# Performance work log

Hardware: AMD Instinct MI355X
Metric: run time of the kernel (lower is better)

## Reference

```python
import jax, jax.numpy as jnp
import numpy as np

LN_EPS = 1e-5

def _prelu(x, a):
    return jnp.where(x > 0, x, a * x)

def setup_inputs() -> dict:
    key = jax.random.key(0)
    ks = jax.random.split(key, 16)
    C, NH, HD = 256, 8, 32
    s = lambda k, shape, scale: jax.random.normal(k, shape, jnp.float32) * scale
    return {
        "x":   s(ks[0], (1, C, 48, 48), 1.0),
        "Wq":  s(ks[1], (NH, HD, C), 1.0 / np.sqrt(C)),
        "bq":  s(ks[2], (NH, HD), 0.02),
        "Wk":  s(ks[3], (NH, HD, C), 1.0 / np.sqrt(C)),
        "bk":  s(ks[4], (NH, HD), 0.02),
        "Wv":  s(ks[5], (NH, HD, C), 1.0 / np.sqrt(C)),
        "bv":  s(ks[6], (NH, HD), 0.02),
        "Wfc": s(ks[7], (C, C), 1.0 / np.sqrt(C)),
        "bfc": s(ks[8], (C,), 0.02),
        "w1":  s(ks[9], (C // 16, C), 1.0 / np.sqrt(C)),
        "b1":  s(ks[10], (C // 16,), 0.02),
        "a1":  jnp.full((1,), 0.25, jnp.float32),
        "w2":  s(ks[11], (C, C // 16), 1.0 / np.sqrt(C // 16)),
        "b2":  s(ks[12], (C,), 0.02),
        "a2":  jnp.full((1,), 0.25, jnp.float32),
    }

def _mha(xs, Wq, bq, Wk, bk, Wv, bv, Wfc, bfc):
    # xs: [B, C, Hs, Ws]; all heads batched into one einsum per projection
    B, C, Hs, Ws = xs.shape
    N = Hs * Ws
    xf = xs.reshape(B, C, N)
    q = jnp.einsum('bcn,hdc->bhnd', xf, Wq) + bq[None, :, None, :]
    k = jnp.einsum('bcn,hdc->bhnd', xf, Wk) + bk[None, :, None, :]
    v = jnp.einsum('bcn,hdc->bhnd', xf, Wv) + bv[None, :, None, :]
    # unscaled scores, softmax over keys (matches torch.bmm(q,k) + softmax dim=-1)
    attn = jax.nn.softmax(jnp.einsum('bhnd,bhmd->bhnm', q, k), axis=-1)
    o = jnp.einsum('bhnm,bhmd->bhnd', attn, v)          # [B, H, N, D]
    o = o.transpose(0, 1, 3, 2).reshape(B, C, Hs, Ws)   # concat heads along C
    return jnp.einsum('bchw,oc->bohw', o, Wfc) + bfc[None, :, None, None]

def reference(x, Wq, bq, Wk, bk, Wv, bv, Wfc, bfc, w1, b1, a1, w2, b2, a2):
    B, C, H, W = x.shape
    num_scales = 4
    out = jnp.zeros_like(x)
    for i in range(num_scales):
        Hs, Ws = H // (2 ** i), W // (2 ** i)
        xs = jax.image.resize(x, (B, C, Hs, Ws), 'bilinear', antialias=False)
        y = _mha(xs, Wq, bq, Wk, bk, Wv, bv, Wfc, bfc)
        out = out + jax.image.resize(y, (B, C, H, W), 'bilinear', antialias=False)
    # SE channel gating
    avg = out.mean(axis=(2, 3))                         # [B, C]
    h = _prelu(avg @ w1.T + b1, a1)
    cw = jax.nn.sigmoid(h @ w2.T + b2)                  # [B, C]
    out = out * cw[:, :, None, None] + x
    # layer_norm over (C, H, W), no affine
    mu = out.mean(axis=(1, 2, 3), keepdims=True)
    var = out.var(axis=(1, 2, 3), keepdims=True)
    out = (out - mu) * jax.lax.rsqrt(var + LN_EPS)
    out = _prelu(out, a2)
    # dropout is identity in eval mode
    return out
```

## Files before the change

kernel.cpp:

```cpp
#include <hip/hip_runtime.h>
#include <hip/hip_bf16.h>

#define NTOT 3060
#define NPIX 2304
#define CH   256
#define NLN  589824
#define VSTR 3072

#define P0_OFF   0
#define P1_OFF   2359296
#define PM0_OFF  2654208
#define PL0_OFF  2727936
#define PM1_OFF  2801664
#define PL1_OFF  2810880

typedef __attribute__((ext_vector_type(8))) short bf16x8;
typedef __attribute__((ext_vector_type(16))) float f32x16;

__device__ __forceinline__ bf16x8 ldfrag(const unsigned short* p) {
  int4 v = *reinterpret_cast<const int4*>(p);
  return __builtin_bit_cast(bf16x8, v);
}
__device__ __forceinline__ unsigned f2bf(float f) {
  unsigned u = __builtin_bit_cast(unsigned, f);
  return (u + 0x7FFFu + ((u >> 16) & 1u)) >> 16;
}
__device__ __forceinline__ unsigned pk2(float a, float b) {
  return f2bf(a) | (f2bf(b) << 16);
}
#define MFMA32(a, b, c) __builtin_amdgcn_mfma_f32_32x32x16_bf16((a), (b), (c), 0, 0, 0)

__global__ __launch_bounds__(256) void k_downsample(const float* __restrict__ x,
                                                    float* __restrict__ xs) {
  int idx = blockIdx.x * 256 + threadIdx.x;
  if (idx >= CH * NTOT) return;
  int c = idx / NTOT;
  int n = idx - c * NTOT;
  const float* xc = x + c * NPIX;
  int p, Ws, s;
  if (n < 2304)      { s = 0; p = n;        Ws = 48; }
  else if (n < 2880) { s = 1; p = n - 2304; Ws = 24; }
  else if (n < 3024) { s = 2; p = n - 2880; Ws = 12; }
  else               { s = 3; p = n - 3024; Ws = 6;  }
  int oy = p / Ws, ox = p - oy * Ws;
  float v;
  if (s == 0) {
    v = xc[p];
  } else {
    int r, cc;
    if (s == 1)      { r = 2 * oy;     cc = 2 * ox;     }
    else if (s == 2) { r = 4 * oy + 1; cc = 4 * ox + 1; }
    else             { r = 8 * oy + 3; cc = 8 * ox + 3; }
    v = 0.25f * (xc[r * 48 + cc] + xc[r * 48 + cc + 1] +
                 xc[(r + 1) * 48 + cc] + xc[(r + 1) * 48 + cc + 1]);
  }
  xs[idx] = v;
}

__global__ __launch_bounds__(256) void k_gemm256(
    const float* __restrict__ A0, const float* __restrict__ A1, const float* __restrict__ A2,
    const float* __restrict__ b0, const float* __restrict__ b1, const float* __restrict__ b2,
    const float* __restrict__ Bm,
    float* __restrict__ O0, float* __restrict__ O1, float* __restrict__ O2) {
  int z = blockIdx.z;
  const float* A    = (z == 0) ? A0 : (z == 1) ? A1 : A2;
  const float* bias = (z == 0) ? b0 : (z == 1) ? b1 : b2;
  float* OUT        = (z == 0) ? O0 : (z == 1) ? O1 : O2;

  __shared__ float As[16][68];
  __shared__ float Bs[16][68];

  int t  = threadIdx.x;
  int j0 = blockIdx.y * 64, n0 = blockIdx.x * 64;
  int ty = t >> 4, tx = t & 15;
  int arow = t >> 2, acol4 = (t & 3) * 4;
  int nn = t & 63, kkb = t >> 6;

  float acc[4][4];
#pragma unroll
  for (int i = 0; i < 4; i++)
#pragma unroll
    for (int q = 0; q < 4; q++) acc[i][q] = 0.f;

  for (int k0 = 0; k0 < 256; k0 += 16) {
    float4 av = *(const float4*)&A[(j0 + arow) * 256 + k0 + acol4];
    float bstage[4];
#pragma unroll
    for (int r = 0; r < 4; r++) {
      int kk = kkb + r * 4;
      int n = n0 + nn;
      bstage[r] = (n < NTOT) ? Bm[(k0 + kk) * NTOT + n] : 0.f;
    }
    __syncthreads();
    As[acol4 + 0][arow] = av.x;
    As[acol4 + 1][arow] = av.y;
    As[acol4 + 2][arow] = av.z;
    As[acol4 + 3][arow] = av.w;
#pragma unroll
    for (int r = 0; r < 4; r++) Bs[kkb + r * 4][nn] = bstage[r];
    __syncthreads();
#pragma unroll
    for (int kk = 0; kk < 16; kk++) {
      float4 a = *(const float4*)&As[kk][ty * 4];
      float4 b = *(const float4*)&Bs[kk][tx * 4];
      float avv[4] = {a.x, a.y, a.z, a.w};
      float bvv[4] = {b.x, b.y, b.z, b.w};
#pragma unroll
      for (int i = 0; i < 4; i++)
#pragma unroll
        for (int q = 0; q < 4; q++) acc[i][q] += avv[i] * bvv[q];
    }
  }
#pragma unroll
  for (int i = 0; i < 4; i++) {
    int j = j0 + ty * 4 + i;
    float bb = bias[j];
#pragma unroll
    for (int q = 0; q < 4; q++) {
      int n = n0 + tx * 4 + q;
      if (n < NTOT) OUT[j * NTOT + n] = acc[i][q] + bb;
    }
  }
}

__global__ __launch_bounds__(256) void k_repackT(const float* __restrict__ Qb,
                                                 const float* __restrict__ Kb,
                                                 unsigned short* __restrict__ Qbf,
                                                 unsigned short* __restrict__ Kbf) {
  __shared__ float Ls[32][65];
  int t = threadIdx.x;
  int n0 = blockIdx.x * 64;
  int h  = blockIdx.y;
  const float* src = (blockIdx.z == 0) ? Qb : Kb;
  unsigned short* dst = (blockIdx.z == 0) ? Qbf : Kbf;
#pragma unroll
  for (int i = 0; i < 8; i++) {
    int idx = t + i * 256;
    int d = idx >> 6, tk = idx & 63;
    int n = n0 + tk;
    Ls[d][tk] = (n < NTOT) ? src[(h * 32 + d) * NTOT + n] : 0.f;
  }
  __syncthreads();
  int tk = t >> 2, dq = t & 3;
  int n = n0 + tk;
  if (n < NTOT) {
    unsigned w[4];
#pragma unroll
    for (int j = 0; j < 4; j++)
      w[j] = pk2(Ls[dq * 8 + 2 * j][tk], Ls[dq * 8 + 2 * j + 1][tk]);
    int4 out = make_int4((int)w[0], (int)w[1], (int)w[2], (int)w[3]);
    *reinterpret_cast<int4*>(&dst[((size_t)h * NTOT + n) * 32 + dq * 8]) = out;
  }
}

__global__ __launch_bounds__(256) void k_castV(const float* __restrict__ Vb,
                                               unsigned short* __restrict__ Vt) {
  int row = blockIdx.x;
  int t = threadIdx.x;
  for (int i = 0; i < 3; i++) {
    int c4 = t + i * 256;
    if (c4 < 765) {
      float4 v = *(const float4*)&Vb[(size_t)row * NTOT + c4 * 4];
      unsigned u0 = pk2(v.x, v.y), u1 = pk2(v.z, v.w);
      int2 out = make_int2((int)u0, (int)u1);
      *reinterpret_cast<int2*>(&Vt[(size_t)row * VSTR + c4 * 4]) = out;
    }
  }
}

__global__ __launch_bounds__(256) void k_attn_mfma(const unsigned short* __restrict__ Qbf,
                                                   const unsigned short* __restrict__ Kbf,
                                                   const unsigned short* __restrict__ Vt,
                                                   float* __restrict__ Ob,
                                                   float* __restrict__ Pb) {
  const int Ns_tab[4]  = {2304, 576, 144, 36};
  const int off_tab[4] = {0, 2304, 2880, 3024};

  int bid = blockIdx.x;
  int sc, head, qt, sp, nsp;
  if (bid < 576)      { int qtb = bid >> 2; sp = bid & 3;  nsp = 4; sc = 0; head = qtb / 18; qt = qtb - head * 18; }
  else if (bid < 656) { int b = bid - 576; int qtb = b >> 1; sp = b & 1; nsp = 2; sc = 1; head = qtb / 5; qt = qtb - head * 5; }
  else if (bid < 672) { int b = bid - 656; sc = 2; head = b >> 1; qt = b & 1; sp = 0; nsp = 1; }
  else                { sc = 3; head = bid - 672; qt = 0; sp = 0; nsp = 1; }

  int Ns = Ns_tab[sc], off = off_tab[sc];
  int t = threadIdx.x;
  int w = t >> 6, l = t & 63;
  int lq = l & 31, h2 = l >> 5;
  int qbase = qt * 128 + w * 32;
  if (qbase >= Ns) return;

  int chunk = Ns / nsp;
  int kbeg = sp * chunk, kend = kbeg + chunk;

  const unsigned short* Qh = Qbf + ((size_t)head * NTOT + off) * 32;
  const unsigned short* Kh = Kbf + ((size_t)head * NTOT + off) * 32;
  const unsigned short* Vh = Vt + (size_t)(head * 32) * VSTR + off;

  int qc = qbase + lq; if (qc >= Ns) qc = Ns - 1;
  const unsigned short* Qp = Qh + (size_t)qc * 32 + h2 * 8;
  bf16x8 qf0 = ldfrag(Qp);
  bf16x8 qf1 = ldfrag(Qp + 16);

  float m = -3.0e38f, L = 0.f;
  f32x16 oacc = {0,0,0,0,0,0,0,0,0,0,0,0,0,0,0,0};

  int mt0 = kbeg + lq; if (mt0 >= Ns) mt0 = Ns - 1;
  const unsigned short* Kp0 = Kh + (size_t)mt0 * 32 + h2 * 8;
  bf16x8 kf0n = ldfrag(Kp0);
  bf16x8 kf1n = ldfrag(Kp0 + 16);

  for (int kb = kbeg; kb < kend; kb += 32) {
    bf16x8 kf0 = kf0n, kf1 = kf1n;
    const unsigned short* Vp = Vh + (size_t)lq * VSTR + kb + h2 * 8;
    bf16x8 vf0 = ldfrag(Vp);
    bf16x8 vf1 = ldfrag(Vp + 16);
    int kb2 = kb + 32;
    if (kb2 < kend) {
      int mt = kb2 + lq; if (mt >= Ns) mt = Ns - 1;
      const unsigned short* Kp = Kh + (size_t)mt * 32 + h2 * 8;
      kf0n = ldfrag(Kp);
      kf1n = ldfrag(Kp + 16);
    }

    f32x16 sa = {0,0,0,0,0,0,0,0,0,0,0,0,0,0,0,0};
    sa = MFMA32(kf0, qf0, sa);
    sa = MFMA32(kf1, qf1, sa);

    float s[16];
#pragma unroll
    for (int r = 0; r < 16; r++) s[r] = sa[r];
    int rem = kend - kb;
    if (rem < 32) {
#pragma unroll
      for (int r = 0; r < 16; r++) {
        int ko = (r & 3) + 8 * (r >> 2) + 4 * h2;
        if (ko >= rem) s[r] = -3.0e38f;
      }
    }
    float cm = s[0];
#pragma unroll
    for (int r = 1; r < 16; r++) cm = fmaxf(cm, s[r]);
    cm = fmaxf(cm, __shfl_xor(cm, 32));
    float mn = fmaxf(m, cm);
    float scl = __expf(m - mn);
    m = mn;
    L *= scl;
#pragma unroll
    for (int r = 0; r < 16; r++) oacc[r] *= scl;

    float p[16], ls = 0.f;
#pragma unroll
    for (int r = 0; r < 16; r++) { p[r] = __expf(s[r] - m); ls += p[r]; }
    ls += __shfl_xor(ls, 32);
    L += ls;

    unsigned u[8], su[8];
#pragma unroll
    for (int g = 0; g < 8; g++) u[g] = pk2(p[2 * g], p[2 * g + 1]);
#pragma unroll
    for (int g = 0; g < 8; g++) su[g] = __shfl_xor(u[g], 32);

    int4 w0, w1;
    if (h2 == 0) {
      w0 = make_int4((int)u[0], (int)u[1], (int)su[0], (int)su[1]);
      w1 = make_int4((int)u[4], (int)u[5], (int)su[4], (int)su[5]);
    } else {
      w0 = make_int4((int)su[2], (int)su[3], (int)u[2], (int)u[3]);
      w1 = make_int4((int)su[6], (int)su[7], (int)u[6], (int)u[7]);
    }
    bf16x8 pf0 = __builtin_bit_cast(bf16x8, w0);
    bf16x8 pf1 = __builtin_bit_cast(bf16x8, w1);

    oacc = MFMA32(vf0, pf0, oacc);
    oacc = MFMA32(vf1, pf1, oacc);
  }

  int q = qbase + lq;
  if (q < Ns) {
    if (nsp == 1) {
      float rl = 1.f / L;
      float* Op = Ob + (size_t)(head * 32) * NTOT + off + q;
#pragma unroll
      for (int r = 0; r < 16; r++) {
        int dr = (r & 3) + 8 * (r >> 2) + 4 * h2;
        Op[(size_t)dr * NTOT] = oacc[r] * rl;
      }
    } else {
      int qs = (sc == 0) ? 2304 : 576;
      float* P  = (sc == 0) ? Pb + P0_OFF  : Pb + P1_OFF;
      float* Pm = (sc == 0) ? Pb + PM0_OFF : Pb + PM1_OFF;
      float* PL = (sc == 0) ? Pb + PL0_OFF : Pb + PL1_OFF;
      size_t row = (size_t)(sp * 8 + head) * qs + q;
      float* Prow = P + row * 32;
#pragma unroll
      for (int g = 0; g < 4; g++) {
        float4 v = make_float4(oacc[4 * g + 0], oacc[4 * g + 1],
                               oacc[4 * g + 2], oacc[4 * g + 3]);
        *(float4*)&Prow[g * 8 + 4 * h2] = v;
      }
      if (h2 == 0) { Pm[row] = m; PL[row] = L; }
    }
  }
}

__global__ __launch_bounds__(256) void k_combine(const float* __restrict__ Pb,
                                                 float* __restrict__ Ob) {
  int tid = blockIdx.x * 256 + threadIdx.x;
  int h, q, off, nsp, qs;
  const float* P; const float* Pm; const float* PL;
  if (tid < 18432) {
    h = tid / 2304; q = tid - h * 2304; off = 0; nsp = 4; qs = 2304;
    P = Pb + P0_OFF; Pm = Pb + PM0_OFF; PL = Pb + PL0_OFF;
  } else if (tid < 23040) {
    int b = tid - 18432;
    h = b / 576; q = b - h * 576; off = 2304; nsp = 2; qs = 576;
    P = Pb + P1_OFF; Pm = Pb + PM1_OFF; PL = Pb + PL1_OFF;
  } else return;

  float mv[4], lv[4];
  float M = -3.0e38f;
  for (int s = 0; s < nsp; s++) {
    size_t row = (size_t)(s * 8 + h) * qs + q;
    mv[s] = Pm[row]; lv[s] = PL[row];
    M = fmaxf(M, mv[s]);
  }
  float e[4], denom = 0.f;
  for (int s = 0; s < nsp; s++) { e[s] = __expf(mv[s] - M); denom += e[s] * lv[s]; }
  float rden = 1.f / denom;

  float* Op = Ob + (size_t)(h * 32) * NTOT + off + q;
#pragma unroll
  for (int d4 = 0; d4 < 8; d4++) {
    float4 acc = make_float4(0.f, 0.f, 0.f, 0.f);
    for (int s = 0; s < nsp; s++) {
      size_t row = (size_t)(s * 8 + h) * qs + q;
      float4 v = *(const float4*)&P[row * 32 + d4 * 4];
      acc.x += e[s] * v.x; acc.y += e[s] * v.y;
      acc.z += e[s] * v.z; acc.w += e[s] * v.w;
    }
    Op[(size_t)(d4 * 4 + 0) * NTOT] = acc.x * rden;
    Op[(size_t)(d4 * 4 + 1) * NTOT] = acc.y * rden;
    Op[(size_t)(d4 * 4 + 2) * NTOT] = acc.z * rden;
    Op[(size_t)(d4 * 4 + 3) * NTOT] = acc.w * rden;
  }
}

__device__ __forceinline__ float bil4(const float* __restrict__ a, int S,
                                      int y, int x, float scale, float tr) {
  float fy = fmaf((float)y, scale, tr);
  float fx = fmaf((float)x, scale, tr);
  int iy = (int)floorf(fy); float wy = fy - (float)iy;
  int ix = (int)floorf(fx); float wx = fx - (float)ix;
  int y0 = min(max(iy, 0), S - 1);
  int y1 = min(max(iy + 1, 0), S - 1);
  int x0 = min(max(ix, 0), S - 1);
  int x1 = min(max(ix + 1, 0), S - 1);
  float v00 = a[y0 * S + x0], v01 = a[y0 * S + x1];
  float v10 = a[y1 * S + x0], v11 = a[y1 * S + x1];
  float top = v00 + wx * (v01 - v00);
  float bot = v10 + wx * (v11 - v10);
  return top + wy * (bot - top);
}

__global__ __launch_bounds__(256) void k_upacc(const float* __restrict__ Y,
                                               float* __restrict__ outa) {
  int idx = blockIdx.x * 256 + threadIdx.x;
  if (idx >= NLN) return;
  int c = idx / NPIX;
  int p = idx - c * NPIX;
  int y = p / 48, x = p - y * 48;
  const float* Yc = Y + c * NTOT;
  float v = Yc[p];
  v += bil4(Yc + 2304, 24, y, x, 0.5f,   -0.25f);
  v += bil4(Yc + 2880, 12, y, x, 0.25f,  -0.375f);
  v += bil4(Yc + 3024, 6,  y, x, 0.125f, -0.4375f);
  outa[idx] = v;
}

__global__ __launch_bounds__(256) void k_chanstats(const float* __restrict__ outa,
                                                   const float* __restrict__ x,
                                                   float* __restrict__ st) {
  int c = blockIdx.x, t = threadIdx.x;
  float so = 0.f, soo = 0.f, sox = 0.f, sx = 0.f, sxx = 0.f;
  for (int p = t; p < NPIX; p += 256) {
    float o  = outa[c * NPIX + p];
    float xv = x[c * NPIX + p];
    so += o; soo += o * o; sox += o * xv; sx += xv; sxx += xv * xv;
  }
#pragma unroll
  for (int off = 32; off > 0; off >>= 1) {
    so  += __shfl_down(so, off, 64);
    soo += __shfl_down(soo, off, 64);
    sox += __shfl_down(sox, off, 64);
    sx  += __shfl_down(sx, off, 64);
    sxx += __shfl_down(sxx, off, 64);
  }
  __shared__ float part[4][5];
  int wv = t >> 6;
  if ((t & 63) == 0) {
    part[wv][0] = so; part[wv][1] = soo; part[wv][2] = sox;
    part[wv][3] = sx; part[wv][4] = sxx;
  }
  __syncthreads();
  if (t == 0) {
    float a0 = 0.f, a1 = 0.f, a2 = 0.f, a3 = 0.f, a4 = 0.f;
#pragma unroll
    for (int wi = 0; wi < 4; wi++) {
      a0 += part[wi][0]; a1 += part[wi][1]; a2 += part[wi][2];
      a3 += part[wi][3]; a4 += part[wi][4];
    }
    st[c] = a0; st[256 + c] = a1; st[512 + c] = a2; st[768 + c] = a3; st[1024 + c] = a4;
  }
}

__global__ __launch_bounds__(256) void k_se(const float* __restrict__ st,
                                            const float* __restrict__ w1,
                                            const float* __restrict__ b1,
                                            const float* __restrict__ a1,
                                            const float* __restrict__ w2,
                                            const float* __restrict__ b2,
                                            float* __restrict__ cw,
                                            float* __restrict__ scal) {
  __shared__ float avg_s[256];
  __shared__ float h_s[16];
  __shared__ float rS[4], rSS[4];
  int t = threadIdx.x;
  float avg = st[t] * (1.f / (float)NPIX);
  avg_s[t] = avg;
  __syncthreads();
  int i = t >> 4, pp = t & 15;
  float partial = 0.f;
  for (int c = pp; c < 256; c += 16) partial += avg_s[c] * w1[i * 256 + c];
#pragma unroll
  for (int off = 8; off > 0; off >>= 1) partial += __shfl_down(partial, off, 16);
  if (pp == 0) {
    float hv = partial + b1[i];
    float al = a1[0];
    h_s[i] = hv > 0.f ? hv : al * hv;
  }
  __syncthreads();
  float s2 = b2[t];
#pragma unroll
  for (int k = 0; k < 16; k++) s2 += h_s[k] * w2[t * 16 + k];
  float cwv = 1.f / (1.f + expf(-s2));
  cw[t] = cwv;

  float S_part  = cwv * st[t] + st[768 + t];
  float SS_part = cwv * cwv * st[256 + t] + 2.f * cwv * st[512 + t] + st[1024 + t];
#pragma unroll
  for (int off = 32; off > 0; off >>= 1) {
    S_part  += __shfl_down(S_part, off, 64);
    SS_part += __shfl_down(SS_part, off, 64);
  }
  if ((t & 63) == 0) { rS[t >> 6] = S_part; rSS[t >> 6] = SS_part; }
  __syncthreads();
  if (t == 0) {
    float S = rS[0] + rS[1] + rS[2] + rS[3];
    float SS = rSS[0] + rSS[1] + rSS[2] + rSS[3];
    float mu = S / (float)NLN;
    float var = SS / (float)NLN - mu * mu;
    scal[0] = mu;
    scal[1] = rsqrtf(var + 1e-5f);
  }
}

__global__ __launch_bounds__(256) void k_final(const float* __restrict__ outa,
                                               const float* __restrict__ x,
                                               const float* __restrict__ cw,
                                               const float* __restrict__ scal,
                                               const float* __restrict__ a2,
                                               float* __restrict__ out) {
  int idx = blockIdx.x * 256 + threadIdx.x;
  if (idx >= NLN) return;
  int c = idx / NPIX;
  float g = outa[idx] * cw[c] + x[idx];
  float v = (g - scal[0]) * scal[1];
  float al = a2[0];
  out[idx] = v > 0.f ? v : al * v;
}

extern "C" void kernel_launch(void* const* d_in, const int* in_sizes, int n_in,
                              void* d_out, int out_size, void* d_ws, size_t ws_size,
                              hipStream_t stream) {
  const float* x   = (const float*)d_in[0];
  const float* Wq  = (const float*)d_in[1];
  const float* bq  = (const float*)d_in[2];
  const float* Wk  = (const float*)d_in[3];
  const float* bk  = (const float*)d_in[4];
  const float* Wv  = (const float*)d_in[5];
  const float* bv  = (const float*)d_in[6];
  const float* Wfc = (const float*)d_in[7];
  const float* bfc = (const float*)d_in[8];
  const float* w1  = (const float*)d_in[9];
  const float* b1  = (const float*)d_in[10];
  const float* a1  = (const float*)d_in[11];
  const float* w2  = (const float*)d_in[12];
  const float* b2  = (const float*)d_in[13];
  const float* a2  = (const float*)d_in[14];

  float* ws   = (float*)d_ws;
  float* xs   = ws;
  float* Qb   = ws + 783360;
  float* Kb   = ws + 1566720;
  float* Vb   = ws + 2350080;
  float* Ob   = ws + 3133440;
  float* Yb   = ws + 3916800;
  float* outa = ws + 4700160;
  float* st   = ws + 5289984;
  float* cwv  = ws + 5291264;
  float* scal = ws + 5291520;

  unsigned short* Qbf = (unsigned short*)(ws + 3916800);
  unsigned short* Kbf = (unsigned short*)(ws + 3916800) + 783360;
  unsigned short* Vt  = (unsigned short*)(ws + 4700160);
  float* Pb = ws;

  k_downsample<<<dim3((CH * NTOT + 255) / 256), 256, 0, stream>>>(x, xs);
  k_gemm256<<<dim3(48, 4, 3), 256, 0, stream>>>(Wq, Wk, Wv, bq, bk, bv, xs, Qb, Kb, Vb);
  k_repackT<<<dim3(48, 8, 2), 256, 0, stream>>>(Qb, Kb, Qbf, Kbf);
  k_castV<<<dim3(256), 256, 0, stream>>>(Vb, Vt);
  k_attn_mfma<<<dim3(680), 256, 0, stream>>>(Qbf, Kbf, Vt, Ob, Pb);
  k_combine<<<dim3(90), 256, 0, stream>>>(Pb, Ob);
  k_gemm256<<<dim3(48, 4, 1), 256, 0, stream>>>(Wfc, Wfc, Wfc, bfc, bfc, bfc, Ob, Yb, Yb, Yb);
  k_upacc<<<dim3(NLN / 256), 256, 0, stream>>>(Yb, outa);
  k_chanstats<<<dim3(256), 256, 0, stream>>>(outa, x, st);
  k_se<<<dim3(1), 256, 0, stream>>>(st, w1, b1, a1, w2, b2, cwv, scal);
  k_final<<<dim3(NLN / 256), 256, 0, stream>>>(outa, x, cwv, scal, a2, (float*)d_out);
}
```

Before: 207.4 us.

## Replace FP32 SIMT projection GEMMs with bf16 MFMA kernels and fused layouts

Replaces the fp32 shared-memory GEMMs for the QKV and output projections with bf16 MFMA kernels. The downsample kernel now writes a transposed bf16 activation, and the QKV kernel writes Q/K/V directly in the bf16 layouts attention consumes, which removes the separate repack and cast kernels. Attention and combine write bf16 output in an [n][C] layout that feeds the FC MFMA kernel. This adds an extra weight-cast kernel and lowers the projection inputs to bf16, which trades some accuracy for fewer launches and faster matrix math.

```diff
diff --git a/kernel.cpp b/kernel.cpp
--- a/kernel.cpp
+++ b/kernel.cpp
@@ -30,140 +30,111 @@
 }
 #define MFMA32(a, b, c) __builtin_amdgcn_mfma_f32_32x32x16_bf16((a), (b), (c), 0, 0, 0)
 
+__global__ __launch_bounds__(256) void k_castW(const float* __restrict__ Wq,
+                                               const float* __restrict__ Wk,
+                                               const float* __restrict__ Wv,
+                                               const float* __restrict__ Wfc,
+                                               unsigned* __restrict__ Wb) {
+  int i = blockIdx.x * 256 + threadIdx.x;
+  int m = i >> 15;
+  int r = i & 32767;
+  const float* src = (m == 0) ? Wq : (m == 1) ? Wk : (m == 2) ? Wv : Wfc;
+  float2 v = *(const float2*)&src[(size_t)r * 2];
+  Wb[i] = pk2(v.x, v.y);
+}
+
 __global__ __launch_bounds__(256) void k_downsample(const float* __restrict__ x,
-                                                    float* __restrict__ xs) {
-  int idx = blockIdx.x * 256 + threadIdx.x;
-  if (idx >= CH * NTOT) return;
-  int c = idx / NTOT;
-  int n = idx - c * NTOT;
-  const float* xc = x + c * NPIX;
+                                                    unsigned short* __restrict__ xsT) {
+  int t = threadIdx.x;
+  int n = blockIdx.x * 64 + (t & 63);
+  int cb = blockIdx.y * 64 + (t >> 6) * 16;
+  if (n >= NTOT) return;
   int p, Ws, s;
   if (n < 2304)      { s = 0; p = n;        Ws = 48; }
   else if (n < 2880) { s = 1; p = n - 2304; Ws = 24; }
   else if (n < 3024) { s = 2; p = n - 2880; Ws = 12; }
   else               { s = 3; p = n - 3024; Ws = 6;  }
   int oy = p / Ws, ox = p - oy * Ws;
-  float v;
-  if (s == 0) {
-    v = xc[p];
-  } else {
+  int b0; bool avg = (s != 0);
+  if (s == 0) b0 = p;
+  else {
     int r, cc;
     if (s == 1)      { r = 2 * oy;     cc = 2 * ox;     }
     else if (s == 2) { r = 4 * oy + 1; cc = 4 * ox + 1; }
     else             { r = 8 * oy + 3; cc = 8 * ox + 3; }
-    v = 0.25f * (xc[r * 48 + cc] + xc[r * 48 + cc + 1] +
-                 xc[(r + 1) * 48 + cc] + xc[(r + 1) * 48 + cc + 1]);
-  }
-  xs[idx] = v;
-}
-
-__global__ __launch_bounds__(256) void k_gemm256(
-    const float* __restrict__ A0, const float* __restrict__ A1, const float* __restrict__ A2,
-    const float* __restrict__ b0, const float* __restrict__ b1, const float* __restrict__ b2,
-    const float* __restrict__ Bm,
-    float* __restrict__ O0, float* __restrict__ O1, float* __restrict__ O2) {
-  int z = blockIdx.z;
-  const float* A    = (z == 0) ? A0 : (z == 1) ? A1 : A2;
-  const float* bias = (z == 0) ? b0 : (z == 1) ? b1 : b2;
-  float* OUT        = (z == 0) ? O0 : (z == 1) ? O1 : O2;
-
-  __shared__ float As[16][68];
-  __shared__ float Bs[16][68];
-
-  int t  = threadIdx.x;
-  int j0 = blockIdx.y * 64, n0 = blockIdx.x * 64;
-  int ty = t >> 4, tx = t & 15;
-  int arow = t >> 2, acol4 = (t & 3) * 4;
-  int nn = t & 63, kkb = t >> 6;
-
-  float acc[4][4];
-#pragma unroll
-  for (int i = 0; i < 4; i++)
-#pragma unroll
-    for (int q = 0; q < 4; q++) acc[i][q] = 0.f;
-
-  for (int k0 = 0; k0 < 256; k0 += 16) {
-    float4 av = *(const float4*)&A[(j0 + arow) * 256 + k0 + acol4];
-    float bstage[4];
-#pragma unroll
-    for (int r = 0; r < 4; r++) {
-      int kk = kkb + r * 4;
-      int n = n0 + nn;
-      bstage[r] = (n < NTOT) ? Bm[(k0 + kk) * NTOT + n] : 0.f;
-    }
-    __syncthreads();
-    As[acol4 + 0][arow] = av.x;
-    As[acol4 + 1][arow] = av.y;
-    As[acol4 + 2][arow] = av.z;
-    As[acol4 + 3][arow] = av.w;
-#pragma unroll
-    for (int r = 0; r < 4; r++) Bs[kkb + r * 4][nn] = bstage[r];
-    __syncthreads();
-#pragma unroll
-    for (int kk = 0; kk < 16; kk++) {
-      float4 a = *(const float4*)&As[kk][ty * 4];
-      float4 b = *(const float4*)&Bs[kk][tx * 4];
-      float avv[4] = {a.x, a.y, a.z, a.w};
-      float bvv[4] = {b.x, b.y, b.z, b.w};
-#pragma unroll
-      for (int i = 0; i < 4; i++)
-#pragma unroll
-        for (int q = 0; q < 4; q++) acc[i][q] += avv[i] * bvv[q];
-    }
-  }
-#pragma unroll
-  for (int i = 0; i < 4; i++) {
-    int j = j0 + ty * 4 + i;
-    float bb = bias[j];
-#pragma unroll
-    for (int q = 0; q < 4; q++) {
-      int n = n0 + tx * 4 + q;
-      if (n < NTOT) OUT[j * NTOT + n] = acc[i][q] + bb;
-    }
-  }
-}
-
-__global__ __launch_bounds__(256) void k_repackT(const float* __restrict__ Qb,
-                                                 const float* __restrict__ Kb,
-                                                 unsigned short* __restrict__ Qbf,
-                                                 unsigned short* __restrict__ Kbf) {
-  __shared__ float Ls[32][65];
-  int t = threadIdx.x;
-  int n0 = blockIdx.x * 64;
-  int h  = blockIdx.y;
-  const float* src = (blockIdx.z == 0) ? Qb : Kb;
-  unsigned short* dst = (blockIdx.z == 0) ? Qbf : Kbf;
-#pragma unroll
-  for (int i = 0; i < 8; i++) {
-    int idx = t + i * 256;
-    int d = idx >> 6, tk = idx & 63;
-    int n = n0 + tk;
-    Ls[d][tk] = (n < NTOT) ? src[(h * 32 + d) * NTOT + n] : 0.f;
-  }
-  __syncthreads();
-  int tk = t >> 2, dq = t & 3;
-  int n = n0 + tk;
+    b0 = r * 48 + cc;
+  }
+#pragma unroll
+  for (int i0 = 0; i0 < 16; i0 += 8) {
+    unsigned u[4];
+#pragma unroll
+    for (int jj = 0; jj < 4; jj++) {
+      float v[2];
+#pragma unroll
+      for (int e = 0; e < 2; e++) {
+        int c = cb + i0 + jj * 2 + e;
+        const float* xc = x + (size_t)c * NPIX;
+        v[e] = avg ? 0.25f * (xc[b0] + xc[b0 + 1] + xc[b0 + 48] + xc[b0 + 49])
+                   : xc[b0];
+      }
+      u[jj] = pk2(v[0], v[1]);
+    }
+    *(int4*)&xsT[(size_t)n * 256 + cb + i0] = make_int4((int)u[0], (int)u[1],
+                                                        (int)u[2], (int)u[3]);
+  }
+}
+
+__global__ __launch_bounds__(256) void k_qkv_mfma(const unsigned short* __restrict__ Wb,
+                                                  const float* __restrict__ bq,
+                                                  const float* __restrict__ bk,
+                                                  const float* __restrict__ bv,
+                                                  const unsigned short* __restrict__ xsT,
+                                                  unsigned short* __restrict__ Qbf,
+                                                  unsigned short* __restrict__ Kbf,
+                                                  unsigned short* __restrict__ Vt) {
+  int z = blockIdx.z, h = blockIdx.y;
+  int j0 = h * 32;
+  const unsigned short* W = Wb + (size_t)z * 65536;
+  const float* bias = (z == 0) ? bq : (z == 1) ? bk : bv;
+  int t = threadIdx.x, w = t >> 6, l = t & 63, lq = l & 31, h2 = l >> 5;
+  int n = blockIdx.x * 128 + w * 32 + lq;
+  int nc = min(n, NTOT - 1);
+
+  bf16x8 bfr[16];
+#pragma unroll
+  for (int kk = 0; kk < 16; kk++)
+    bfr[kk] = ldfrag(&xsT[(size_t)nc * 256 + kk * 16 + h2 * 8]);
+
+  f32x16 acc = {0,0,0,0,0,0,0,0,0,0,0,0,0,0,0,0};
+#pragma unroll
+  for (int kk = 0; kk < 16; kk++) {
+    bf16x8 af = ldfrag(&W[(size_t)(j0 + lq) * 256 + kk * 16 + h2 * 8]);
+    acc = MFMA32(af, bfr[kk], acc);
+  }
+
+  float4 bi[4];
+#pragma unroll
+  for (int g = 0; g < 4; g++) bi[g] = *(const float4*)&bias[j0 + 4 * h2 + 8 * g];
+
   if (n < NTOT) {
-    unsigned w[4];
-#pragma unroll
-    for (int j = 0; j < 4; j++)
-      w[j] = pk2(Ls[dq * 8 + 2 * j][tk], Ls[dq * 8 + 2 * j + 1][tk]);
-    int4 out = make_int4((int)w[0], (int)w[1], (int)w[2], (int)w[3]);
-    *reinterpret_cast<int4*>(&dst[((size_t)h * NTOT + n) * 32 + dq * 8]) = out;
-  }
-}
-
-__global__ __launch_bounds__(256) void k_castV(const float* __restrict__ Vb,
-                                               unsigned short* __restrict__ Vt) {
-  int row = blockIdx.x;
-  int t = threadIdx.x;
-  for (int i = 0; i < 3; i++) {
-    int c4 = t + i * 256;
-    if (c4 < 765) {
-      float4 v = *(const float4*)&Vb[(size_t)row * NTOT + c4 * 4];
-      unsigned u0 = pk2(v.x, v.y), u1 = pk2(v.z, v.w);
-      int2 out = make_int2((int)u0, (int)u1);
-      *reinterpret_cast<int2*>(&Vt[(size_t)row * VSTR + c4 * 4]) = out;
+    if (z < 2) {
+      unsigned short* dst = ((z == 0) ? Qbf : Kbf) + ((size_t)h * NTOT + n) * 32;
+#pragma unroll
+      for (int g = 0; g < 4; g++) {
+        unsigned p0 = pk2(acc[4 * g + 0] + bi[g].x, acc[4 * g + 1] + bi[g].y);
+        unsigned p1 = pk2(acc[4 * g + 2] + bi[g].z, acc[4 * g + 3] + bi[g].w);
+        *(int2*)&dst[4 * h2 + 8 * g] = make_int2((int)p0, (int)p1);
+      }
+    } else {
+#pragma unroll
+      for (int g = 0; g < 4; g++) {
+        float bb[4] = {bi[g].x, bi[g].y, bi[g].z, bi[g].w};
+#pragma unroll
+        for (int q = 0; q < 4; q++) {
+          int d = 4 * h2 + 8 * g + q;
+          Vt[(size_t)(j0 + d) * VSTR + n] = (unsigned short)f2bf(acc[4 * g + q] + bb[q]);
+        }
+      }
     }
   }
 }
@@ -171,7 +142,7 @@
 __global__ __launch_bounds__(256) void k_attn_mfma(const unsigned short* __restrict__ Qbf,
                                                    const unsigned short* __restrict__ Kbf,
                                                    const unsigned short* __restrict__ Vt,
-                                                   float* __restrict__ Ob,
+                                                   unsigned short* __restrict__ Obf,
                                                    float* __restrict__ Pb) {
   const int Ns_tab[4]  = {2304, 576, 144, 36};
   const int off_tab[4] = {0, 2304, 2880, 3024};
@@ -280,11 +251,12 @@
   if (q < Ns) {
     if (nsp == 1) {
       float rl = 1.f / L;
-      float* Op = Ob + (size_t)(head * 32) * NTOT + off + q;
-#pragma unroll
-      for (int r = 0; r < 16; r++) {
-        int dr = (r & 3) + 8 * (r >> 2) + 4 * h2;
-        Op[(size_t)dr * NTOT] = oacc[r] * rl;
+      unsigned short* dst = Obf + (size_t)(off + q) * 256 + head * 32;
+#pragma unroll
+      for (int g = 0; g < 4; g++) {
+        unsigned p0 = pk2(oacc[4 * g + 0] * rl, oacc[4 * g + 1] * rl);
+        unsigned p1 = pk2(oacc[4 * g + 2] * rl, oacc[4 * g + 3] * rl);
+        *(int2*)&dst[4 * h2 + 8 * g] = make_int2((int)p0, (int)p1);
       }
     } else {
       int qs = (sc == 0) ? 2304 : 576;
@@ -305,7 +277,7 @@
 }
 
 __global__ __launch_bounds__(256) void k_combine(const float* __restrict__ Pb,
-                                                 float* __restrict__ Ob) {
+                                                 unsigned short* __restrict__ Obf) {
   int tid = blockIdx.x * 256 + threadIdx.x;
   int h, q, off, nsp, qs;
   const float* P; const float* Pm; const float* PL;
@@ -329,7 +301,7 @@
   for (int s = 0; s < nsp; s++) { e[s] = __expf(mv[s] - M); denom += e[s] * lv[s]; }
   float rden = 1.f / denom;
 
-  float* Op = Ob + (size_t)(h * 32) * NTOT + off + q;
+  unsigned short* dst = Obf + (size_t)(off + q) * 256 + h * 32;
 #pragma unroll
   for (int d4 = 0; d4 < 8; d4++) {
     float4 acc = make_float4(0.f, 0.f, 0.f, 0.f);
@@ -339,10 +311,47 @@
       acc.x += e[s] * v.x; acc.y += e[s] * v.y;
       acc.z += e[s] * v.z; acc.w += e[s] * v.w;
     }
-    Op[(size_t)(d4 * 4 + 0) * NTOT] = acc.x * rden;
-    Op[(size_t)(d4 * 4 + 1) * NTOT] = acc.y * rden;
-    Op[(size_t)(d4 * 4 + 2) * NTOT] = acc.z * rden;
-    Op[(size_t)(d4 * 4 + 3) * NTOT] = acc.w * rden;
+    unsigned p0 = pk2(acc.x * rden, acc.y * rden);
+    unsigned p1 = pk2(acc.z * rden, acc.w * rden);
+    *(int2*)&dst[d4 * 4] = make_int2((int)p0, (int)p1);
+  }
+}
+
+__global__ __launch_bounds__(256) void k_fc_mfma(const unsigned short* __restrict__ Wfcb,
+                                                 const float* __restrict__ bfc,
+                                                 const unsigned short* __restrict__ Obf,
+                                                 float* __restrict__ Yb) {
+  int j0 = blockIdx.y * 32;
+  int t = threadIdx.x, w = t >> 6, l = t & 63, lq = l & 31, h2 = l >> 5;
+  int n = blockIdx.x * 128 + w * 32 + lq;
+  int nc = min(n, NTOT - 1);
+
+  bf16x8 bfr[16];
+#pragma unroll
+  for (int kk = 0; kk < 16; kk++)
+    bfr[kk] = ldfrag(&Obf[(size_t)nc * 256 + kk * 16 + h2 * 8]);
+
+  f32x16 acc = {0,0,0,0,0,0,0,0,0,0,0,0,0,0,0,0};
+#pragma unroll
+  for (int kk = 0; kk < 16; kk++) {
+    bf16x8 af = ldfrag(&Wfcb[(size_t)(j0 + lq) * 256 + kk * 16 + h2 * 8]);
+    acc = MFMA32(af, bfr[kk], acc);
+  }
+
+  float4 bi[4];
+#pragma unroll
+  for (int g = 0; g < 4; g++) bi[g] = *(const float4*)&bfc[j0 + 4 * h2 + 8 * g];
+
+  if (n < NTOT) {
+#pragma unroll
+    for (int g = 0; g < 4; g++) {
+      float bb[4] = {bi[g].x, bi[g].y, bi[g].z, bi[g].w};
+#pragma unroll
+      for (int q = 0; q < 4; q++) {
+        int d = 4 * h2 + 8 * g + q;
+        Yb[(size_t)(j0 + d) * NTOT + n] = acc[4 * g + q] + bb[q];
+      }
+    }
   }
 }
 
@@ -499,30 +508,26 @@
   const float* b2  = (const float*)d_in[13];
   const float* a2  = (const float*)d_in[14];
 
-  float* ws   = (float*)d_ws;
-  float* xs   = ws;
-  float* Qb   = ws + 783360;
-  float* Kb   = ws + 1566720;
-  float* Vb   = ws + 2350080;
-  float* Ob   = ws + 3133440;
-  float* Yb   = ws + 3916800;
+  float* ws = (float*)d_ws;
+  unsigned short* xsT = (unsigned short*)ws;
+  float* Pb = ws;
+  unsigned short* Obf = (unsigned short*)(ws + 3133440);
+  unsigned short* Wb  = (unsigned short*)(ws + 3525120);
+  unsigned short* Qbf = (unsigned short*)(ws + 3916800);
+  unsigned short* Kbf = Qbf + 783360;
+  float* Yb = ws + 3916800;
+  unsigned short* Vt = (unsigned short*)(ws + 4700160);
   float* outa = ws + 4700160;
   float* st   = ws + 5289984;
   float* cwv  = ws + 5291264;
   float* scal = ws + 5291520;
 
-  unsigned short* Qbf = (unsigned short*)(ws + 3916800);
-  unsigned short* Kbf = (unsigned short*)(ws + 3916800) + 783360;
-  unsigned short* Vt  = (unsigned short*)(ws + 4700160);
-  float* Pb = ws;
-
-  k_downsample<<<dim3((CH * NTOT + 255) / 256), 256, 0, stream>>>(x, xs);
-  k_gemm256<<<dim3(48, 4, 3), 256, 0, stream>>>(Wq, Wk, Wv, bq, bk, bv, xs, Qb, Kb, Vb);
-  k_repackT<<<dim3(48, 8, 2), 256, 0, stream>>>(Qb, Kb, Qbf, Kbf);
-  k_castV<<<dim3(256), 256, 0, stream>>>(Vb, Vt);
-  k_attn_mfma<<<dim3(680), 256, 0, stream>>>(Qbf, Kbf, Vt, Ob, Pb);
-  k_combine<<<dim3(90), 256, 0, stream>>>(Pb, Ob);
-  k_gemm256<<<dim3(48, 4, 1), 256, 0, stream>>>(Wfc, Wfc, Wfc, bfc, bfc, bfc, Ob, Yb, Yb, Yb);
+  k_castW<<<dim3(512), 256, 0, stream>>>(Wq, Wk, Wv, Wfc, (unsigned*)Wb);
+  k_downsample<<<dim3(48, 4), 256, 0, stream>>>(x, xsT);
+  k_qkv_mfma<<<dim3(24, 8, 3), 256, 0, stream>>>(Wb, bq, bk, bv, xsT, Qbf, Kbf, Vt);
+  k_attn_mfma<<<dim3(680), 256, 0, stream>>>(Qbf, Kbf, Vt, Obf, Pb);
+  k_combine<<<dim3(90), 256, 0, stream>>>(Pb, Obf);
+  k_fc_mfma<<<dim3(24, 8), 256, 0, stream>>>(Wb + 196608, bfc, Obf, Yb);
   k_upacc<<<dim3(NLN / 256), 256, 0, stream>>>(Yb, outa);
   k_chanstats<<<dim3(256), 256, 0, stream>>>(outa, x, st);
   k_se<<<dim3(1), 256, 0, stream>>>(st, w1, b1, a1, w2, b2, cwv, scal);
```

Result: faster. 173.5 us (-16.3%).
